# Optimization experiments

Hardware: AMD Instinct MI355X
Metric: run time of the kernel (lower is better)

The kernel has to match this reference:

```python
import jax, jax.numpy as jnp
import numpy as np

TOPK = 8
EPS = 1e-12  # F.normalize eps


def setup_inputs() -> dict:
    key = jax.random.key(0)
    k1, k2 = jax.random.split(key)
    feats = jax.random.normal(k1, (4, 256, 64, 64), dtype=jnp.float32)
    logits = jax.random.normal(k2, (4, 1, 64, 64), dtype=jnp.float32)
    return {"feats": feats, "logits": logits}


def reference(feats, logits):
    b, c, h, w = feats.shape
    n = h * w
    feat_flat = feats.reshape(b, c, n)
    # F.normalize(dim=1): x / max(||x||_2, eps)
    norm = jnp.sqrt(jnp.sum(feat_flat * feat_flat, axis=1, keepdims=True))
    feat_norm = feat_flat / jnp.maximum(norm, EPS)
    # sim[b,i,j] = <f_i, f_j>  -> [B, N, N]
    sim = jnp.einsum('bci,bcj->bij', feat_norm, feat_norm)
    k = min(TOPK, n)
    _, idx = jax.lax.top_k(sim, k)  # [B, N, k] indices
    prob = jax.nn.sigmoid(logits).reshape(b, n)  # [B, N]
    # gathered[b,i,j] = prob[b, idx[b,i,j]]
    gathered = jax.vmap(lambda p, i: p[i])(prob, idx)  # [B, N, k]
    anchor = prob[:, :, None]  # [B, N, 1] broadcast over k
    loss = jnp.mean(jnp.abs(anchor - gathered))
    return loss
```

## Files before the change

### kernel.cpp

```cpp
#include <hip/hip_runtime.h>
#include <hip/hip_bf16.h>

typedef _Float16 half8 __attribute__((ext_vector_type(8)));
typedef unsigned short ushort8 __attribute__((ext_vector_type(8)));
typedef float floatx4 __attribute__((ext_vector_type(4)));

#define B_ 4
#define C_ 256
#define N_ 4096
#define NT 32
#define TRI 528

#define OFF_FN    ((size_t)0)
#define OFF_PROB  ((size_t)(8u << 20))
#define OFF_PART  (OFF_PROB + 65536)
#define OFF_TOP   ((size_t)(16u << 20))

__device__ __forceinline__ void gl_lds16(const void* g, void* l) {
    __builtin_amdgcn_global_load_lds(
        (const __attribute__((address_space(1))) void*)g,
        (__attribute__((address_space(3))) void*)l,
        16, 0, 0);
}

__device__ __forceinline__ unsigned short flip16(float v) {
    uint32_t bits = (uint32_t)__builtin_bit_cast(unsigned short, (_Float16)v);
    return (unsigned short)(bits ^ (((bits >> 15) * 0x7FFFu) + 0x8000u));
}

__device__ __forceinline__ void cas(uint32_t& a, uint32_t& b) {
    uint32_t hi = max(a, b); b = min(a, b); a = hi;
}

__device__ __forceinline__ void sort8(uint32_t v[8]) {
    cas(v[0],v[1]); cas(v[2],v[3]); cas(v[4],v[5]); cas(v[6],v[7]);
    cas(v[0],v[2]); cas(v[1],v[3]); cas(v[4],v[6]); cas(v[5],v[7]);
    cas(v[1],v[2]); cas(v[5],v[6]);
    cas(v[0],v[4]); cas(v[1],v[5]); cas(v[2],v[6]); cas(v[3],v[7]);
    cas(v[2],v[4]); cas(v[3],v[5]);
    cas(v[1],v[2]); cas(v[3],v[4]); cas(v[5],v[6]);
}

__device__ __forceinline__ void merge8(uint32_t r[8], const uint32_t n[8]) {
    uint32_t m[8];
#pragma unroll
    for (int i = 0; i < 8; ++i) m[i] = max(r[i], n[7 - i]);
    cas(m[0],m[4]); cas(m[1],m[5]); cas(m[2],m[6]); cas(m[3],m[7]);
    cas(m[0],m[2]); cas(m[1],m[3]); cas(m[4],m[6]); cas(m[5],m[7]);
    cas(m[0],m[1]); cas(m[2],m[3]); cas(m[4],m[5]); cas(m[6],m[7]);
#pragma unroll
    for (int i = 0; i < 8; ++i) r[i] = m[i];
}

#define TS 68
__global__ __launch_bounds__(256) void prep_kernel(const float* __restrict__ feats,
                                                   const float* __restrict__ logits,
                                                   _Float16* __restrict__ fn,
                                                   float* __restrict__ prob) {
    __shared__ __align__(16) float T[C_ * TS];
    __shared__ float S[256];
    __shared__ float I[64];

    const int t  = threadIdx.x;
    const int b  = blockIdx.x >> 6;
    const int i0 = (blockIdx.x & 63) * 64;
    const float* fb = feats + (size_t)b * C_ * N_;

#pragma unroll
    for (int k = 0; k < 16; ++k) {
        int ch = t + k * 256;
        int row = ch >> 4, col4 = ch & 15;
        float4 v = *(const float4*)(fb + (size_t)row * N_ + i0 + col4 * 4);
        *(float4*)&T[row * TS + col4 * 4] = v;
    }
    __syncthreads();
    {
        int i = t & 63, cq = t >> 6;
        float ss = 0.f;
#pragma unroll 8
        for (int j = 0; j < 64; ++j) { float v = T[(cq * 64 + j) * TS + i]; ss += v * v; }
        S[cq * 64 + i] = ss;
    }
    __syncthreads();
    if (t < 64) {
        float ss = S[t] + S[64 + t] + S[128 + t] + S[192 + t];
        I[t] = 1.f / fmaxf(sqrtf(ss), 1e-12f);
        float lg = logits[b * N_ + i0 + t];
        prob[b * N_ + i0 + t] = 1.f / (1.f + expf(-lg));
    }
    __syncthreads();
    {
        int i = t >> 2, chunk = t & 3;
        float s = I[i];
        _Float16* fr = fn + ((size_t)(b * N_ + i0 + i)) * C_ + chunk * 64;
#pragma unroll
        for (int v8 = 0; v8 < 8; ++v8) {
            half8 h;
#pragma unroll
            for (int e = 0; e < 8; ++e)
                h[e] = (_Float16)(T[(chunk * 64 + v8 * 8 + e) * TS + i] * s);
            *(half8*)(fr + v8 * 8) = h;
        }
    }
}

#define CSH 132
__global__ __launch_bounds__(256) void gram_sel_kernel(const _Float16* __restrict__ fn,
                                                       uint32_t* __restrict__ top) {
    __shared__ __align__(16) char smem[128 * CSH * 2];
    _Float16* As = (_Float16*)smem;
    _Float16* Bs = (_Float16*)(smem + 16384);
    unsigned short* Ch = (unsigned short*)smem;
    uint32_t* Ms = (uint32_t*)smem;

    const int t    = threadIdx.x;
    const int lane = t & 63;
    const int w    = t >> 6;
    const int m16  = lane & 15;
    const int q    = lane >> 4;

    const int b = blockIdx.x / TRI;
    const int u = blockIdx.x - b * TRI;
    int it = (int)(32.5f - sqrtf(32.5f * 32.5f - 2.0f * (float)u));
    while (u >= (it + 1) * (65 - (it + 1)) / 2) ++it;
    while (u < it * (65 - it) / 2) --it;
    const int jt = it + (u - it * (65 - it) / 2);
    const bool diag = (it == jt);

    const int i0 = it * 128, j0 = jt * 128;
    const _Float16* fnb = fn + (size_t)b * N_ * C_;

    const int srowb = t >> 3;
    const int schunk = (t & 7) ^ (srowb & 7);
    const int sw = m16 & 7;

    floatx4 acc[2][8];
#pragma unroll
    for (int ri = 0; ri < 2; ++ri)
#pragma unroll
        for (int jj = 0; jj < 8; ++jj) acc[ri][jj] = floatx4{0.f, 0.f, 0.f, 0.f};

    for (int kc = 0; kc < 4; ++kc) {
#pragma unroll
        for (int r = 0; r < 4; ++r) {
            int row = r * 32 + srowb;
            const _Float16* gA = fnb + (size_t)(i0 + row) * C_ + kc * 64 + schunk * 8;
            const _Float16* gB = fnb + (size_t)(j0 + row) * C_ + kc * 64 + schunk * 8;
            gl_lds16(gA, (char*)As + r * 4096 + t * 16);
            gl_lds16(gB, (char*)Bs + r * 4096 + t * 16);
        }
        __syncthreads();
#pragma unroll
        for (int kk = 0; kk < 2; ++kk) {
            half8 a0 = *(const half8*)&As[(w * 32 + m16) * 64 + ((kk * 4 + q) ^ sw) * 8];
            half8 a1 = *(const half8*)&As[(w * 32 + 16 + m16) * 64 + ((kk * 4 + q) ^ sw) * 8];
#pragma unroll
            for (int jj = 0; jj < 8; ++jj) {
                half8 bf = *(const half8*)&Bs[(jj * 16 + m16) * 64 + ((kk * 4 + q) ^ sw) * 8];
                acc[0][jj] = __builtin_amdgcn_mfma_f32_16x16x32_f16(a0, bf, acc[0][jj], 0, 0, 0);
                acc[1][jj] = __builtin_amdgcn_mfma_f32_16x16x32_f16(a1, bf, acc[1][jj], 0, 0, 0);
            }
        }
        __syncthreads();
    }

#pragma unroll
    for (int jj = 0; jj < 8; ++jj)
#pragma unroll
        for (int ri = 0; ri < 2; ++ri)
#pragma unroll
            for (int r = 0; r < 4; ++r) {
                int row = w * 32 + ri * 16 + q * 4 + r;
                Ch[row * CSH + jj * 16 + m16] = flip16(acc[ri][jj][r]);
            }
    __syncthreads();

    uint32_t rowpk[8], colpk[8];
    {
        const int rrow = t >> 1, rc0 = (t & 1) * 64;
        const unsigned short* cr = &Ch[rrow * CSH + rc0];
        const int jbase = j0 + rc0;
#pragma unroll
        for (int g = 0; g < 8; ++g) {
            ushort8 v = *(const ushort8*)(cr + g * 8);
            uint32_t cand[8];
#pragma unroll
            for (int e = 0; e < 8; ++e)
                cand[e] = ((uint32_t)v[e] << 16) | (uint32_t)(jbase + g * 8 + e);
            sort8(cand);
            if (g == 0) {
#pragma unroll
                for (int s = 0; s < 8; ++s) rowpk[s] = cand[s];
            } else merge8(rowpk, cand);
        }
    }
    if (!diag) {
        const int ccol = t >> 1, cr0 = (t & 1) * 64;
        const unsigned short* cc = &Ch[cr0 * CSH + ccol];
        const int ibase = i0 + cr0;
#pragma unroll
        for (int g = 0; g < 8; ++g) {
            uint32_t cand[8];
#pragma unroll
            for (int e = 0; e < 8; ++e)
                cand[e] = ((uint32_t)cc[(g * 8 + e) * CSH] << 16) | (uint32_t)(ibase + g * 8 + e);
            sort8(cand);
            if (g == 0) {
#pragma unroll
                for (int s = 0; s < 8; ++s) colpk[s] = cand[s];
            } else merge8(colpk, cand);
        }
    }
    __syncthreads();

    if (t & 1) {
#pragma unroll
        for (int s = 0; s < 8; ++s) Ms[(t >> 1) * 8 + s] = rowpk[s];
        if (!diag) {
#pragma unroll
            for (int s = 0; s < 8; ++s) Ms[1024 + (t >> 1) * 8 + s] = colpk[s];
        }
    }
    __syncthreads();
    if (!(t & 1)) {
        uint32_t o[8];
#pragma unroll
        for (int s = 0; s < 8; ++s) o[s] = Ms[(t >> 1) * 8 + s];
        merge8(rowpk, o);
        uint32_t* dst = top + (((size_t)b * N_ + i0 + (t >> 1)) * 32 + jt) * 8;
        *(uint4*)dst       = make_uint4(rowpk[0], rowpk[1], rowpk[2], rowpk[3]);
        *(uint4*)(dst + 4) = make_uint4(rowpk[4], rowpk[5], rowpk[6], rowpk[7]);
        if (!diag) {
#pragma unroll
            for (int s = 0; s < 8; ++s) o[s] = Ms[1024 + (t >> 1) * 8 + s];
            merge8(colpk, o);
            uint32_t* dst2 = top + (((size_t)b * N_ + j0 + (t >> 1)) * 32 + it) * 8;
            *(uint4*)dst2       = make_uint4(colpk[0], colpk[1], colpk[2], colpk[3]);
            *(uint4*)(dst2 + 4) = make_uint4(colpk[4], colpk[5], colpk[6], colpk[7]);
        }
    }
}

__global__ __launch_bounds__(256) void merge_kernel(const uint32_t* __restrict__ top,
                                                    const float* __restrict__ prob,
                                                    float* __restrict__ partials) {
    __shared__ float red[4];
    const int t = threadIdx.x;
    const int lane = t & 63;
    const int w = t >> 6;
    const int rg = blockIdx.x * 4 + w;
    const int b = rg >> 12;

    uint4 v4 = ((const uint4*)(top + (size_t)rg * 256))[lane];
    uint32_t v[4] = {v4.x, v4.y, v4.z, v4.w};
    uint32_t m = max(max(v[0], v[1]), max(v[2], v[3]));

    const float* pb = prob + (b << 12);
    float p_r = prob[rg];
    float contrib = 0.f;
#pragma unroll
    for (int k = 0; k < 8; ++k) {
        uint32_t M = m;
#pragma unroll
        for (int off = 32; off; off >>= 1) M = max(M, (uint32_t)__shfl_xor((int)M, off));
        if (lane == k) contrib = fabsf(p_r - pb[M & 0xFFFu]);
#pragma unroll
        for (int s = 0; s < 4; ++s) v[s] = (v[s] == M) ? 0u : v[s];
        m = max(max(v[0], v[1]), max(v[2], v[3]));
    }
#pragma unroll
    for (int off = 32; off; off >>= 1) contrib += __shfl_xor(contrib, off);
    if (lane == 0) red[w] = contrib;
    __syncthreads();
    if (t == 0) partials[blockIdx.x] = red[0] + red[1] + red[2] + red[3];
}

__global__ __launch_bounds__(256) void final_kernel(const float* __restrict__ partials,
                                                    float* __restrict__ out) {
    __shared__ float red[256];
    int t = threadIdx.x;
    float s = 0.f;
#pragma unroll
    for (int k = 0; k < 16; ++k) s += partials[k * 256 + t];
    red[t] = s;
    __syncthreads();
    for (int off = 128; off > 0; off >>= 1) {
        if (t < off) red[t] += red[t + off];
        __syncthreads();
    }
    if (t == 0) out[0] = red[0] * (1.f / (B_ * N_ * 8.0f));
}

extern "C" void kernel_launch(void* const* d_in, const int* in_sizes, int n_in,
                              void* d_out, int out_size, void* d_ws, size_t ws_size,
                              hipStream_t stream) {
    const float* feats  = (const float*)d_in[0];
    const float* logits = (const float*)d_in[1];
    float* out = (float*)d_out;
    char* ws = (char*)d_ws;
    _Float16* fn   = (_Float16*)(ws + OFF_FN);
    float* prob    = (float*)(ws + OFF_PROB);
    float* parts   = (float*)(ws + OFF_PART);
    uint32_t* top  = (uint32_t*)(ws + OFF_TOP);

    prep_kernel<<<256, 256, 0, stream>>>(feats, logits, fn, prob);
    gram_sel_kernel<<<B_ * TRI, 256, 0, stream>>>(fn, top);
    merge_kernel<<<4096, 256, 0, stream>>>(top, prob, parts);
    final_kernel<<<1, 256, 0, stream>>>(parts, out);
}
```

Before: 137.1 us.

## Transpose Gram tile store with packed fp16 flips and fuse final reduction

The Gram tile epilogue now writes the sim tile into LDS transposed, converting two accumulators per packed fp16 store (cvt_pkrtz) with a vectorized order-preserving flip, so that the column-wise top-8 scan reads contiguously. Row and column roles swap, and the LDS stride changes to 136. An occupancy hint of 3 waves is added via launch_bounds. The separate final reduction kernel is removed: merge_kernel uses a global atomic counter, reset in prep_kernel, so the last block sums all partials, saving one launch at the cost of an atomic per block and a memory-ordering dependency.

```diff
diff --git a/kernel.cpp b/kernel.cpp
--- a/kernel.cpp
+++ b/kernel.cpp
@@ -14,6 +14,7 @@
 #define OFF_FN    ((size_t)0)
 #define OFF_PROB  ((size_t)(8u << 20))
 #define OFF_PART  (OFF_PROB + 65536)
+#define OFF_CNT   (OFF_PART + 16384)
 #define OFF_TOP   ((size_t)(16u << 20))
 
 __device__ __forceinline__ void gl_lds16(const void* g, void* l) {
@@ -21,11 +22,6 @@
         (const __attribute__((address_space(1))) void*)g,
         (__attribute__((address_space(3))) void*)l,
         16, 0, 0);
-}
-
-__device__ __forceinline__ unsigned short flip16(float v) {
-    uint32_t bits = (uint32_t)__builtin_bit_cast(unsigned short, (_Float16)v);
-    return (unsigned short)(bits ^ (((bits >> 15) * 0x7FFFu) + 0x8000u));
 }
 
 __device__ __forceinline__ void cas(uint32_t& a, uint32_t& b) {
@@ -56,7 +52,8 @@
 __global__ __launch_bounds__(256) void prep_kernel(const float* __restrict__ feats,
                                                    const float* __restrict__ logits,
                                                    _Float16* __restrict__ fn,
-                                                   float* __restrict__ prob) {
+                                                   float* __restrict__ prob,
+                                                   uint32_t* __restrict__ counter) {
     __shared__ __align__(16) float T[C_ * TS];
     __shared__ float S[256];
     __shared__ float I[64];
@@ -65,6 +62,7 @@
     const int b  = blockIdx.x >> 6;
     const int i0 = (blockIdx.x & 63) * 64;
     const float* fb = feats + (size_t)b * C_ * N_;
+    if (blockIdx.x == 0 && t == 0) *counter = 0u;
 
 #pragma unroll
     for (int k = 0; k < 16; ++k) {
@@ -104,9 +102,9 @@
     }
 }
 
-#define CSH 132
-__global__ __launch_bounds__(256) void gram_sel_kernel(const _Float16* __restrict__ fn,
-                                                       uint32_t* __restrict__ top) {
+#define CSH 136
+__global__ __launch_bounds__(256, 3) void gram_sel_kernel(const _Float16* __restrict__ fn,
+                                                          uint32_t* __restrict__ top) {
     __shared__ __align__(16) char smem[128 * CSH * 2];
     _Float16* As = (_Float16*)smem;
     _Float16* Bs = (_Float16*)(smem + 16384);
@@ -167,58 +165,64 @@
 #pragma unroll
     for (int jj = 0; jj < 8; ++jj)
 #pragma unroll
-        for (int ri = 0; ri < 2; ++ri)
-#pragma unroll
-            for (int r = 0; r < 4; ++r) {
-                int row = w * 32 + ri * 16 + q * 4 + r;
-                Ch[row * CSH + jj * 16 + m16] = flip16(acc[ri][jj][r]);
+        for (int ri = 0; ri < 2; ++ri) {
+            const int col = jj * 16 + m16;
+            const int row = w * 32 + ri * 16 + q * 4;
+#pragma unroll
+            for (int p = 0; p < 2; ++p) {
+                auto pk2 = __builtin_amdgcn_cvt_pkrtz(acc[ri][jj][2 * p], acc[ri][jj][2 * p + 1]);
+                uint32_t bits = __builtin_bit_cast(uint32_t, pk2);
+                uint32_t s = (bits >> 15) & 0x00010001u;
+                uint32_t fl = bits ^ (s * 0x7FFFu + 0x80008000u);
+                *(uint32_t*)&Ch[col * CSH + row + 2 * p] = fl;
             }
-    __syncthreads();
-
-    uint32_t rowpk[8], colpk[8];
+        }
+    __syncthreads();
+
+    uint32_t cpk[8], rpk[8];
     {
-        const int rrow = t >> 1, rc0 = (t & 1) * 64;
-        const unsigned short* cr = &Ch[rrow * CSH + rc0];
-        const int jbase = j0 + rc0;
+        const int ccol = t >> 1, cr0 = (t & 1) * 64;
+        const unsigned short* cc = &Ch[ccol * CSH + cr0];
+        const int ibase = i0 + cr0;
 #pragma unroll
         for (int g = 0; g < 8; ++g) {
-            ushort8 v = *(const ushort8*)(cr + g * 8);
+            ushort8 v = *(const ushort8*)(cc + g * 8);
             uint32_t cand[8];
 #pragma unroll
             for (int e = 0; e < 8; ++e)
-                cand[e] = ((uint32_t)v[e] << 16) | (uint32_t)(jbase + g * 8 + e);
+                cand[e] = ((uint32_t)v[e] << 16) | (uint32_t)(ibase + g * 8 + e);
             sort8(cand);
             if (g == 0) {
 #pragma unroll
-                for (int s = 0; s < 8; ++s) rowpk[s] = cand[s];
-            } else merge8(rowpk, cand);
+                for (int s = 0; s < 8; ++s) cpk[s] = cand[s];
+            } else merge8(cpk, cand);
         }
     }
     if (!diag) {
-        const int ccol = t >> 1, cr0 = (t & 1) * 64;
-        const unsigned short* cc = &Ch[cr0 * CSH + ccol];
-        const int ibase = i0 + cr0;
+        const int rrow = t >> 1, ch0 = (t & 1) * 64;
+        const unsigned short* cr = &Ch[ch0 * CSH + rrow];
+        const int jbase = j0 + ch0;
 #pragma unroll
         for (int g = 0; g < 8; ++g) {
             uint32_t cand[8];
 #pragma unroll
             for (int e = 0; e < 8; ++e)
-                cand[e] = ((uint32_t)cc[(g * 8 + e) * CSH] << 16) | (uint32_t)(ibase + g * 8 + e);
+                cand[e] = ((uint32_t)cr[(g * 8 + e) * CSH] << 16) | (uint32_t)(jbase + g * 8 + e);
             sort8(cand);
             if (g == 0) {
 #pragma unroll
-                for (int s = 0; s < 8; ++s) colpk[s] = cand[s];
-            } else merge8(colpk, cand);
+                for (int s = 0; s < 8; ++s) rpk[s] = cand[s];
+            } else merge8(rpk, cand);
         }
     }
     __syncthreads();
 
     if (t & 1) {
 #pragma unroll
-        for (int s = 0; s < 8; ++s) Ms[(t >> 1) * 8 + s] = rowpk[s];
+        for (int s = 0; s < 8; ++s) Ms[(t >> 1) * 8 + s] = cpk[s];
         if (!diag) {
 #pragma unroll
-            for (int s = 0; s < 8; ++s) Ms[1024 + (t >> 1) * 8 + s] = colpk[s];
+            for (int s = 0; s < 8; ++s) Ms[1024 + (t >> 1) * 8 + s] = rpk[s];
         }
     }
     __syncthreads();
@@ -226,25 +230,29 @@
         uint32_t o[8];
 #pragma unroll
         for (int s = 0; s < 8; ++s) o[s] = Ms[(t >> 1) * 8 + s];
-        merge8(rowpk, o);
-        uint32_t* dst = top + (((size_t)b * N_ + i0 + (t >> 1)) * 32 + jt) * 8;
-        *(uint4*)dst       = make_uint4(rowpk[0], rowpk[1], rowpk[2], rowpk[3]);
-        *(uint4*)(dst + 4) = make_uint4(rowpk[4], rowpk[5], rowpk[6], rowpk[7]);
+        merge8(cpk, o);
+        uint32_t* dst = top + (((size_t)b * N_ + j0 + (t >> 1)) * 32 + it) * 8;
+        *(uint4*)dst       = make_uint4(cpk[0], cpk[1], cpk[2], cpk[3]);
+        *(uint4*)(dst + 4) = make_uint4(cpk[4], cpk[5], cpk[6], cpk[7]);
         if (!diag) {
 #pragma unroll
             for (int s = 0; s < 8; ++s) o[s] = Ms[1024 + (t >> 1) * 8 + s];
-            merge8(colpk, o);
-            uint32_t* dst2 = top + (((size_t)b * N_ + j0 + (t >> 1)) * 32 + it) * 8;
-            *(uint4*)dst2       = make_uint4(colpk[0], colpk[1], colpk[2], colpk[3]);
-            *(uint4*)(dst2 + 4) = make_uint4(colpk[4], colpk[5], colpk[6], colpk[7]);
+            merge8(rpk, o);
+            uint32_t* dst2 = top + (((size_t)b * N_ + i0 + (t >> 1)) * 32 + jt) * 8;
+            *(uint4*)dst2       = make_uint4(rpk[0], rpk[1], rpk[2], rpk[3]);
+            *(uint4*)(dst2 + 4) = make_uint4(rpk[4], rpk[5], rpk[6], rpk[7]);
         }
     }
 }
 
 __global__ __launch_bounds__(256) void merge_kernel(const uint32_t* __restrict__ top,
                                                     const float* __restrict__ prob,
-                                                    float* __restrict__ partials) {
+                                                    float* __restrict__ partials,
+                                                    uint32_t* __restrict__ counter,
+                                                    float* __restrict__ out) {
     __shared__ float red[4];
+    __shared__ float red2[256];
+    __shared__ int lastFlag;
     const int t = threadIdx.x;
     const int lane = t & 63;
     const int w = t >> 6;
@@ -272,23 +280,26 @@
     for (int off = 32; off; off >>= 1) contrib += __shfl_xor(contrib, off);
     if (lane == 0) red[w] = contrib;
     __syncthreads();
-    if (t == 0) partials[blockIdx.x] = red[0] + red[1] + red[2] + red[3];
-}
-
-__global__ __launch_bounds__(256) void final_kernel(const float* __restrict__ partials,
-                                                    float* __restrict__ out) {
-    __shared__ float red[256];
-    int t = threadIdx.x;
-    float s = 0.f;
-#pragma unroll
-    for (int k = 0; k < 16; ++k) s += partials[k * 256 + t];
-    red[t] = s;
-    __syncthreads();
-    for (int off = 128; off > 0; off >>= 1) {
-        if (t < off) red[t] += red[t + off];
+    if (t == 0) {
+        float p = red[0] + red[1] + red[2] + red[3];
+        __hip_atomic_store(&partials[blockIdx.x], p, __ATOMIC_RELAXED, __HIP_MEMORY_SCOPE_AGENT);
+        uint32_t old = __hip_atomic_fetch_add(counter, 1u, __ATOMIC_ACQ_REL, __HIP_MEMORY_SCOPE_AGENT);
+        lastFlag = (old == 4095u);
+    }
+    __syncthreads();
+    if (lastFlag) {
+        float s = 0.f;
+#pragma unroll
+        for (int k = 0; k < 16; ++k)
+            s += __hip_atomic_load(&partials[k * 256 + t], __ATOMIC_RELAXED, __HIP_MEMORY_SCOPE_AGENT);
+        red2[t] = s;
         __syncthreads();
-    }
-    if (t == 0) out[0] = red[0] * (1.f / (B_ * N_ * 8.0f));
+        for (int off = 128; off > 0; off >>= 1) {
+            if (t < off) red2[t] += red2[t + off];
+            __syncthreads();
+        }
+        if (t == 0) out[0] = red2[0] * (1.f / (B_ * N_ * 8.0f));
+    }
 }
 
 extern "C" void kernel_launch(void* const* d_in, const int* in_sizes, int n_in,
@@ -301,10 +312,10 @@
     _Float16* fn   = (_Float16*)(ws + OFF_FN);
     float* prob    = (float*)(ws + OFF_PROB);
     float* parts   = (float*)(ws + OFF_PART);
+    uint32_t* cnt  = (uint32_t*)(ws + OFF_CNT);
     uint32_t* top  = (uint32_t*)(ws + OFF_TOP);
 
-    prep_kernel<<<256, 256, 0, stream>>>(feats, logits, fn, prob);
+    prep_kernel<<<256, 256, 0, stream>>>(feats, logits, fn, prob, cnt);
     gram_sel_kernel<<<B_ * TRI, 256, 0, stream>>>(fn, top);
-    merge_kernel<<<4096, 256, 0, stream>>>(top, prob, parts);
-    final_kernel<<<1, 256, 0, stream>>>(parts, out);
-}
+    merge_kernel<<<4096, 256, 0, stream>>>(top, prob, parts, cnt, out);
+}
```

Measured after the change: 202.8 us. +47.9%, slower.
